# Kernel tuning notes

Measured on AMD Instinct MI355X. Metric: run time of the kernel, lower is better.

## Reference

```python
import jax, jax.numpy as jnp
import numpy as np

NUM_GRAPHS = 16  # static number of graphs for pooling
BN_EPS = 1e-5


def gat_layer(x, W, a_src, a_dst, src, dst, N, concat):
    # x: (N, Fin), W: (H, Fin, Fout), a_src/a_dst: (H, Fout)
    Wh = jnp.einsum('ni,hio->hno', x, W)                      # (H, N, Fout)
    e_src = jnp.einsum('hno,ho->hn', Wh, a_src)               # (H, N)
    e_dst = jnp.einsum('hno,ho->hn', Wh, a_dst)               # (H, N)
    e = jax.nn.leaky_relu(e_src[:, src] + e_dst[:, dst], 0.2)  # (H, E)
    # edge softmax over incoming edges per dst; torch code starts max at 0
    seg_max = jax.vmap(lambda eh: jax.ops.segment_max(eh, dst, num_segments=N))(e)
    e_max = jnp.maximum(seg_max, 0.0)                         # (H, N)
    exp_e = jnp.exp(e - e_max[:, dst])                        # (H, E)
    exp_sum = jax.vmap(lambda eh: jax.ops.segment_sum(eh, dst, num_segments=N))(exp_e)
    attn = exp_e / (exp_sum[:, dst] + 1e-8)                   # (H, E)
    msgs = attn[:, :, None] * Wh[:, src]                      # (H, E, Fout)
    out = jax.vmap(lambda m: jax.ops.segment_sum(m, dst, num_segments=N))(msgs)  # (H, N, Fout)
    if concat:
        out = jnp.transpose(out, (1, 0, 2)).reshape(N, -1)
    else:
        out = out.mean(axis=0)
    return out, attn


def batchnorm(h, gamma, beta):
    mu = h.mean(axis=0)
    var = h.var(axis=0)
    return (h - mu) / jnp.sqrt(var + BN_EPS) * gamma + beta


def setup_inputs() -> dict:
    key = jax.random.key(0)
    ks = jax.random.split(key, 20)
    N, E = 50000, 400000
    IN, HID, H, NC = 262, 128, 4, 2

    def xavier(k, shape):
        fan_in, fan_out = shape[-2], shape[-1]
        lim = np.sqrt(6.0 / (fan_in + fan_out))
        return jax.random.uniform(k, shape, jnp.float32, -lim, lim)

    x = jax.random.normal(ks[0], (N, IN), jnp.float32)
    edge_index = jax.random.randint(ks[1], (2, E), 0, N, jnp.int64)
    batch = jnp.sort(jax.random.randint(ks[2], (N,), 0, NUM_GRAPHS, jnp.int64))

    return {
        'x': x, 'edge_index': edge_index, 'batch': batch,
        'W1': xavier(ks[3], (H, IN, HID)),
        'a_src1': xavier(ks[4], (H, HID, 1)).squeeze(-1),
        'a_dst1': xavier(ks[5], (H, HID, 1)).squeeze(-1),
        'W2': xavier(ks[6], (1, HID * H, HID)),
        'a_src2': xavier(ks[7], (1, HID, 1)).squeeze(-1),
        'a_dst2': xavier(ks[8], (1, HID, 1)).squeeze(-1),
        'bn1_g': jnp.ones((HID * H,), jnp.float32),
        'bn1_b': jnp.zeros((HID * H,), jnp.float32),
        'bn2_g': jnp.ones((HID,), jnp.float32),
        'bn2_b': jnp.zeros((HID,), jnp.float32),
        'cls_w1': xavier(ks[9], (HID, HID // 2)),
        'cls_b1': jnp.zeros((HID // 2,), jnp.float32),
        'cls_w2': xavier(ks[10], (HID // 2, NC)),
        'cls_b2': jnp.zeros((NC,), jnp.float32),
        'ep_w1': xavier(ks[11], (HID * 2, HID)),
        'ep_b1': jnp.zeros((HID,), jnp.float32),
        'ep_w2': xavier(ks[12], (HID, 1)),
        'ep_b2': jnp.zeros((1,), jnp.float32),
    }


def reference(x, edge_index, batch, W1, a_src1, a_dst1, W2, a_src2, a_dst2,
              bn1_g, bn1_b, bn2_g, bn2_b, cls_w1, cls_b1, cls_w2, cls_b2,
              ep_w1, ep_b1, ep_w2, ep_b2):
    N = x.shape[0]
    src, dst = edge_index[0], edge_index[1]

    h1, _ = gat_layer(x, W1, a_src1, a_dst1, src, dst, N, concat=True)
    h1 = batchnorm(jax.nn.elu(h1), bn1_g, bn1_b)

    h2, attn2 = gat_layer(h1, W2, a_src2, a_dst2, src, dst, N, concat=False)
    h2 = batchnorm(jax.nn.elu(h2), bn2_g, bn2_b)

    # global mean pool over graphs
    sums = jax.ops.segment_sum(h2, batch, num_segments=NUM_GRAPHS)
    counts = jax.ops.segment_sum(jnp.ones((N,), h2.dtype), batch, num_segments=NUM_GRAPHS)
    graph_repr = sums / jnp.clip(counts, 1.0)[:, None]

    logits = jax.nn.relu(graph_repr @ cls_w1 + cls_b1) @ cls_w2 + cls_b2

    edge_feat = jnp.concatenate([h2[src], h2[dst]], axis=1)  # (E, 2*hidden)
    importance = jax.nn.sigmoid(
        (jax.nn.relu(edge_feat @ ep_w1 + ep_b1) @ ep_w2 + ep_b2).squeeze(-1))

    gat_attention = jnp.transpose(attn2, (1, 0))  # (E, 1)
    return logits, h2, importance, gat_attention
```

## Files before the change

### kernel.cpp

```cpp
#include <hip/hip_runtime.h>
#include <hip/hip_bf16.h>
#include <math.h>

typedef __hip_bfloat16 bf16;
typedef __bf16 bf16x8 __attribute__((ext_vector_type(8)));
typedef __bf16 bf16x2v __attribute__((ext_vector_type(2)));
typedef float f32x4 __attribute__((ext_vector_type(4)));

#define NN 50000
#define EE 400000
#define FIN 262
#define KP1 288
#define HID 128
#define NH 4
#define C1 512
#define NGR 16
#define SCAN_NB ((NN + 255) / 256)

__device__ __forceinline__ float b2f(bf16 x){ return __bfloat162float(x); }
__device__ __forceinline__ bf16 f2b(float x){ return __float2bfloat16(x); }
__device__ __forceinline__ float lrelu(float v){ return v >= 0.f ? v : 0.2f * v; }

__global__ void zero_words(unsigned int* __restrict__ p, int n) {
  int i = blockIdx.x * 256 + threadIdx.x;
  if (i < n) p[i] = 0u;
}

__global__ __launch_bounds__(256)
void gemm_mfma(const bf16* __restrict__ A, const bf16* __restrict__ Bt,
               bf16* __restrict__ C, int M, int K, int Ncols) {
  __shared__ __align__(16) __bf16 As[128 * 40];
  __shared__ __align__(16) __bf16 Bs[128 * 40];
  int bm = blockIdx.y * 128, bn = blockIdx.x * 128;
  int tid = threadIdx.x;
  int wave = tid >> 6, lane = tid & 63;
  int quad = lane >> 4, l16 = lane & 15;
  int wm = (wave >> 1) * 64, wn = (wave & 1) * 64;
  f32x4 acc[4][4];
  #pragma unroll
  for (int i = 0; i < 4; ++i)
    #pragma unroll
    for (int j = 0; j < 4; ++j)
      acc[i][j] = (f32x4){0.f, 0.f, 0.f, 0.f};

  for (int k0 = 0; k0 < K; k0 += 32) {
    #pragma unroll
    for (int l = 0; l < 2; ++l) {
      int e = l * 2048 + tid * 8;
      int row = e >> 5, col = e & 31;
      uint4 va = {0u, 0u, 0u, 0u};
      int gm = bm + row;
      if (gm < M) va = *(const uint4*)(A + (size_t)gm * K + k0 + col);
      *(uint4*)(&As[row * 40 + col]) = va;
      uint4 vb = {0u, 0u, 0u, 0u};
      int gn = bn + row;
      if (gn < Ncols) vb = *(const uint4*)(Bt + (size_t)gn * K + k0 + col);
      *(uint4*)(&Bs[row * 40 + col]) = vb;
    }
    __syncthreads();
    bf16x8 af[4], bf_[4];
    #pragma unroll
    for (int i = 0; i < 4; ++i)
      af[i] = *(const bf16x8*)(&As[(wm + i * 16 + l16) * 40 + quad * 8]);
    #pragma unroll
    for (int j = 0; j < 4; ++j)
      bf_[j] = *(const bf16x8*)(&Bs[(wn + j * 16 + l16) * 40 + quad * 8]);
    #pragma unroll
    for (int i = 0; i < 4; ++i)
      #pragma unroll
      for (int j = 0; j < 4; ++j)
        acc[i][j] = __builtin_amdgcn_mfma_f32_16x16x32_bf16(af[i], bf_[j], acc[i][j], 0, 0, 0);
    __syncthreads();
  }
  #pragma unroll
  for (int i = 0; i < 4; ++i) {
    #pragma unroll
    for (int r = 0; r < 4; ++r) {
      int gm = bm + wm + i * 16 + quad * 4 + r;
      if (gm >= M) continue;
      #pragma unroll
      for (int j = 0; j < 4; ++j) {
        int gn = bn + wn + j * 16 + l16;
        C[(size_t)gm * Ncols + gn] = f2b(acc[i][j][r]);
      }
    }
  }
}

__global__ void conv_x(const float* __restrict__ x, bf16* __restrict__ xb) {
  int i = blockIdx.x * 256 + threadIdx.x;
  if (i >= NN * KP1) return;
  int row = i / KP1, col = i - row * KP1;
  xb[i] = (col < FIN) ? f2b(x[(size_t)row * FIN + col]) : f2b(0.f);
}
__global__ void prep_b1t(const float* __restrict__ W1, bf16* __restrict__ B1t) {
  int i = blockIdx.x * 256 + threadIdx.x;
  if (i >= C1 * KP1) return;
  int n = i / KP1, k = i - n * KP1;
  int h = n >> 7, o = n & 127;
  B1t[i] = (k < FIN) ? f2b(W1[((size_t)h * FIN + k) * HID + o]) : f2b(0.f);
}
__global__ void prep_b2t(const float* __restrict__ W2, bf16* __restrict__ B2t) {
  int i = blockIdx.x * 256 + threadIdx.x;
  if (i >= HID * C1) return;
  int n = i >> 9, k = i & 511;
  B2t[i] = f2b(W2[(size_t)k * HID + n]);
}
__global__ void prep_bpt(const float* __restrict__ epw1, bf16* __restrict__ BPt) {
  int i = blockIdx.x * 256 + threadIdx.x;
  if (i >= 256 * HID) return;
  int n = i >> 7, k = i & 127;
  float v = (n < 128) ? epw1[(size_t)k * HID + n] : epw1[(size_t)(128 + k) * HID + (n - 128)];
  BPt[i] = f2b(v);
}

__global__ void edot_all(const bf16* __restrict__ Wh1, const float* __restrict__ av,
                         const float* __restrict__ bv, float* __restrict__ es1,
                         float* __restrict__ ed1) {
  int wid = threadIdx.x >> 6, lane = threadIdx.x & 63;
  int n = blockIdx.x * 4 + wid;
  if (n >= NN) return;
  int h = lane >> 4, c16 = lane & 15;
  int fbase = h * HID + c16 * 8;
  bf16x8 r = *(const bf16x8*)(Wh1 + (size_t)n * C1 + fbase);
  float s1 = 0.f, s2 = 0.f;
  #pragma unroll
  for (int j = 0; j < 8; ++j) {
    float rv = (float)r[j];
    s1 += rv * av[fbase + j];
    s2 += rv * bv[fbase + j];
  }
  #pragma unroll
  for (int off = 8; off > 0; off >>= 1) {
    s1 += __shfl_xor(s1, off);
    s2 += __shfl_xor(s2, off);
  }
  if (c16 == 0) { es1[n * 4 + h] = s1; ed1[n * 4 + h] = s2; }
}

__global__ void edot1(const bf16* __restrict__ Wh, const float* __restrict__ av,
                      const float* __restrict__ bv, float* __restrict__ es,
                      float* __restrict__ ed) {
  int wid = threadIdx.x >> 6, lane = threadIdx.x & 63;
  int r = blockIdx.x * 4 + wid;
  if (r >= NN) return;
  const bf16* row = Wh + (size_t)r * HID;
  float w0 = b2f(row[lane]), w1 = b2f(row[lane + 64]);
  float s1 = w0 * av[lane] + w1 * av[lane + 64];
  float s2 = w0 * bv[lane] + w1 * bv[lane + 64];
  #pragma unroll
  for (int off = 32; off > 0; off >>= 1) {
    s1 += __shfl_xor(s1, off);
    s2 += __shfl_xor(s2, off);
  }
  if (lane == 0) { es[r] = s1; ed[r] = s2; }
}

__global__ void count_kernel(const int* __restrict__ dst, int* __restrict__ deg, int E) {
  int e = blockIdx.x * blockDim.x + threadIdx.x;
  if (e >= E) return;
  int d = dst[e];
  if ((unsigned)d < NN) atomicAdd(&deg[d], 1);
}

__global__ void scan_p1(const int* __restrict__ deg, int* __restrict__ bsum) {
  __shared__ int s[256];
  int t = threadIdx.x;
  int i = blockIdx.x * 256 + t;
  s[t] = (i < NN) ? deg[i] : 0;
  __syncthreads();
  #pragma unroll
  for (int off = 128; off > 0; off >>= 1) {
    if (t < off) s[t] += s[t + off];
    __syncthreads();
  }
  if (t == 0) bsum[blockIdx.x] = s[0];
}
__global__ void scan_p2(const int* __restrict__ bsum, int* __restrict__ boff,
                        int* __restrict__ total_out) {
  __shared__ int s[256];
  int t = threadIdx.x;
  s[t] = (t < SCAN_NB) ? bsum[t] : 0;
  __syncthreads();
  if (t == 0) {
    int r = 0;
    for (int i = 0; i < SCAN_NB; ++i) { int v = s[i]; s[i] = r; r += v; }
    total_out[0] = r;
  }
  __syncthreads();
  if (t < SCAN_NB) boff[t] = s[t];
}
__global__ void scan_p3(const int* __restrict__ deg, const int* __restrict__ boff,
                        int* __restrict__ rowptr, int* __restrict__ cursor) {
  __shared__ int s[256];
  int t = threadIdx.x;
  int i = blockIdx.x * 256 + t;
  int v = (i < NN) ? deg[i] : 0;
  s[t] = v;
  __syncthreads();
  #pragma unroll
  for (int off = 1; off < 256; off <<= 1) {
    int add = (t >= off) ? s[t - off] : 0;
    __syncthreads();
    s[t] += add;
    __syncthreads();
  }
  if (i < NN) {
    int pos = boff[blockIdx.x] + s[t] - v;
    rowptr[i] = pos;
    cursor[i] = pos;
  }
}

__global__ void scatter_kernel(const int* __restrict__ src, const int* __restrict__ dst,
                               int* __restrict__ cursor, int* __restrict__ csr_s,
                               int* __restrict__ csr_d, int* __restrict__ csr_e, int E) {
  int e = blockIdx.x * blockDim.x + threadIdx.x;
  if (e >= E) return;
  int d = dst[e];
  if ((unsigned)d >= NN) return;
  int s = src[e]; if ((unsigned)s >= NN) s = 0;
  int p = atomicAdd(&cursor[d], 1);
  if ((unsigned)p < (unsigned)E) { csr_s[p] = s; csr_d[p] = d; csr_e[p] = e; }
}

__global__ void logits1(const int* __restrict__ csr_s, const int* __restrict__ csr_d,
                        const float4* __restrict__ es1, const float4* __restrict__ ed1,
                        float4* __restrict__ v1, int* __restrict__ m1i) {
  int j = blockIdx.x * 256 + threadIdx.x;
  if (j >= EE) return;
  int s = csr_s[j]; if ((unsigned)s >= NN) s = 0;
  int d = csr_d[j]; if ((unsigned)d >= NN) d = 0;
  float4 a = es1[s], bb = ed1[d];
  float4 v;
  v.x = lrelu(a.x + bb.x);
  v.y = lrelu(a.y + bb.y);
  v.z = lrelu(a.z + bb.z);
  v.w = lrelu(a.w + bb.w);
  v1[j] = v;
  if (v.x > 0.f) atomicMax(&m1i[d * 4 + 0], __float_as_int(v.x));
  if (v.y > 0.f) atomicMax(&m1i[d * 4 + 1], __float_as_int(v.y));
  if (v.z > 0.f) atomicMax(&m1i[d * 4 + 2], __float_as_int(v.z));
  if (v.w > 0.f) atomicMax(&m1i[d * 4 + 3], __float_as_int(v.w));
}

__global__ void logits2(const int* __restrict__ csr_s, const int* __restrict__ csr_d,
                        const float* __restrict__ es2, const float* __restrict__ ed2,
                        float* __restrict__ v2, int* __restrict__ m2i) {
  int j = blockIdx.x * 256 + threadIdx.x;
  if (j >= EE) return;
  int s = csr_s[j]; if ((unsigned)s >= NN) s = 0;
  int d = csr_d[j]; if ((unsigned)d >= NN) d = 0;
  float v = lrelu(es2[s] + ed2[d]);
  v2[j] = v;
  if (v > 0.f) atomicMax(&m2i[d], __float_as_int(v));
}

__global__ __launch_bounds__(256, 6)
void agg1_all(const int* __restrict__ csr_s, const int* __restrict__ rowptr,
              const float* __restrict__ lg, const float* __restrict__ mx,
              const bf16* __restrict__ Wh1, bf16* __restrict__ h1) {
  int wid = threadIdx.x >> 6, lane = threadIdx.x & 63;
  int node = blockIdx.x * 4 + wid;
  if (node >= NN) return;
  int b = rowptr[node], e = rowptr[node + 1];
  if (b < 0) b = 0; if (e > EE) e = EE;
  int h = lane >> 4;
  float m = mx[node * 4 + h];
  float sum = 0.f;
  float acc[8] = {};
  int j = b;
  for (; j + 4 <= e; j += 4) {
    int s0 = csr_s[j], s1 = csr_s[j + 1], s2 = csr_s[j + 2], s3 = csr_s[j + 3];
    float w0 = lg[(j + 0) * 4 + h], w1 = lg[(j + 1) * 4 + h],
          w2 = lg[(j + 2) * 4 + h], w3 = lg[(j + 3) * 4 + h];
    bf16x8 r0 = *(const bf16x8*)(Wh1 + (size_t)s0 * C1 + lane * 8);
    bf16x8 r1 = *(const bf16x8*)(Wh1 + (size_t)s1 * C1 + lane * 8);
    bf16x8 r2 = *(const bf16x8*)(Wh1 + (size_t)s2 * C1 + lane * 8);
    bf16x8 r3 = *(const bf16x8*)(Wh1 + (size_t)s3 * C1 + lane * 8);
    float p0 = __expf(w0 - m), p1 = __expf(w1 - m);
    float p2 = __expf(w2 - m), p3 = __expf(w3 - m);
    sum += (p0 + p1) + (p2 + p3);
    #pragma unroll
    for (int k = 0; k < 8; ++k)
      acc[k] += (p0 * (float)r0[k] + p1 * (float)r1[k]) +
                (p2 * (float)r2[k] + p3 * (float)r3[k]);
  }
  for (; j < e; ++j) {
    int s0 = csr_s[j];
    float w0 = lg[j * 4 + h];
    bf16x8 r0 = *(const bf16x8*)(Wh1 + (size_t)s0 * C1 + lane * 8);
    float p0 = __expf(w0 - m);
    sum += p0;
    #pragma unroll
    for (int k = 0; k < 8; ++k) acc[k] += p0 * (float)r0[k];
  }
  float scale = 1.f / (sum + 1e-8f);
  bf16x8 o;
  #pragma unroll
  for (int k = 0; k < 8; ++k) o[k] = (__bf16)(acc[k] * scale);
  *(bf16x8*)(h1 + (size_t)node * C1 + lane * 8) = o;
}

__global__ __launch_bounds__(256, 8)
void agg2_all(const int* __restrict__ csr_s, const int* __restrict__ rowptr,
              const float* __restrict__ lg, const float* __restrict__ mx,
              const bf16* __restrict__ Wh2, bf16* __restrict__ h2p,
              float* __restrict__ invs2) {
  int wid = threadIdx.x >> 6, lane = threadIdx.x & 63;
  int node = blockIdx.x * 4 + wid;
  if (node >= NN) return;
  int b = rowptr[node], e = rowptr[node + 1];
  if (b < 0) b = 0; if (e > EE) e = EE;
  float m = mx[node];
  float sum = 0.f, a0 = 0.f, a1 = 0.f;
  int j = b;
  for (; j + 4 <= e; j += 4) {
    int s0 = csr_s[j], s1 = csr_s[j + 1], s2 = csr_s[j + 2], s3 = csr_s[j + 3];
    float w0 = lg[j], w1 = lg[j + 1], w2 = lg[j + 2], w3 = lg[j + 3];
    bf16x2v r0 = *(const bf16x2v*)(Wh2 + (size_t)s0 * HID + lane * 2);
    bf16x2v r1 = *(const bf16x2v*)(Wh2 + (size_t)s1 * HID + lane * 2);
    bf16x2v r2 = *(const bf16x2v*)(Wh2 + (size_t)s2 * HID + lane * 2);
    bf16x2v r3 = *(const bf16x2v*)(Wh2 + (size_t)s3 * HID + lane * 2);
    float p0 = __expf(w0 - m), p1 = __expf(w1 - m);
    float p2 = __expf(w2 - m), p3 = __expf(w3 - m);
    sum += (p0 + p1) + (p2 + p3);
    a0 += (p0 * (float)r0[0] + p1 * (float)r1[0]) + (p2 * (float)r2[0] + p3 * (float)r3[0]);
    a1 += (p0 * (float)r0[1] + p1 * (float)r1[1]) + (p2 * (float)r2[1] + p3 * (float)r3[1]);
  }
  for (; j < e; ++j) {
    int s0 = csr_s[j];
    float w0 = lg[j];
    bf16x2v r0 = *(const bf16x2v*)(Wh2 + (size_t)s0 * HID + lane * 2);
    float p0 = __expf(w0 - m);
    sum += p0;
    a0 += p0 * (float)r0[0];
    a1 += p0 * (float)r0[1];
  }
  float scale = 1.f / (sum + 1e-8f);
  bf16x2v o;
  o[0] = (__bf16)(a0 * scale);
  o[1] = (__bf16)(a1 * scale);
  *(bf16x2v*)(h2p + (size_t)node * HID + lane * 2) = o;
  if (lane == 0) invs2[node] = scale;
}

__global__ void attn_csr(const int* __restrict__ csr_d, const int* __restrict__ csr_e,
                         const float* __restrict__ lg, const float* __restrict__ mx,
                         const float* __restrict__ invs2, float* __restrict__ out) {
  int j = blockIdx.x * 256 + threadIdx.x;
  if (j >= EE) return;
  int d = csr_d[j]; if ((unsigned)d >= NN) d = 0;
  int e = csr_e[j]; if ((unsigned)e >= EE) return;
  out[e] = __expf(lg[j] - mx[d]) * invs2[d];
}

__global__ void elu_stats(bf16* __restrict__ X, float* __restrict__ cs, float* __restrict__ cq,
                          int Nrows, int C) {
  int c = threadIdx.x;
  int rpb = (Nrows + gridDim.x - 1) / gridDim.x;
  int r0 = blockIdx.x * rpb, r1 = min(r0 + rpb, Nrows);
  float s = 0.f, s2 = 0.f;
  for (int r = r0; r < r1; ++r) {
    size_t idx = (size_t)r * C + c;
    float v = b2f(X[idx]);
    v = v > 0.f ? v : expm1f(v);
    X[idx] = f2b(v);
    s += v; s2 += v * v;
  }
  atomicAdd(&cs[c], s);
  atomicAdd(&cq[c], s2);
}

__global__ void bn_apply(const bf16* __restrict__ in, bf16* __restrict__ out,
                         float* __restrict__ out2,
                         const float* __restrict__ cs, const float* __restrict__ cq,
                         const float* __restrict__ gamma, const float* __restrict__ beta,
                         int C, size_t total, float invN) {
  size_t i = (size_t)blockIdx.x * blockDim.x + threadIdx.x;
  if (i >= total) return;
  int c = (int)(i % C);
  float mu = cs[c] * invN;
  float var = cq[c] * invN - mu * mu;
  float v = (b2f(in[i]) - mu) * rsqrtf(fmaxf(var, 0.f) + 1e-5f) * gamma[c] + beta[c];
  out[i] = f2b(v);
  if (out2) out2[i] = v;
}

__global__ __launch_bounds__(256)
void pool_kernel(const bf16* __restrict__ h2, const int* __restrict__ batch,
                 float* __restrict__ pooled) {
  int t = threadIdx.x;
  int f = t & 127, half = t >> 7;
  int r0 = blockIdx.x * 32;
  int g_cur = -1;
  float acc = 0.f;
  #pragma unroll
  for (int i = 0; i < 16; ++i) {
    int r = r0 + half + 2 * i;
    if (r >= NN) break;
    int g = batch[r]; if ((unsigned)g >= NGR) g = 0;
    float v = b2f(h2[(size_t)r * HID + f]);
    if (g != g_cur) {
      if (g_cur >= 0) atomicAdd(&pooled[g_cur * HID + f], acc);
      g_cur = g; acc = 0.f;
    }
    acc += v;
  }
  if (g_cur >= 0) atomicAdd(&pooled[g_cur * HID + f], acc);
}

__global__ void cnt_kernel(const int* __restrict__ batch, float* __restrict__ cnt) {
  int g = threadIdx.x;
  if (g >= NGR) return;
  int a = 0, b = NN;
  while (a < b) { int m = (a + b) >> 1; if (batch[m] < g) a = m + 1; else b = m; }
  int lb = a;
  a = 0; b = NN;
  while (a < b) { int m = (a + b) >> 1; if (batch[m] <= g) a = m + 1; else b = m; }
  cnt[g] = (float)(a - lb);
}

__global__ void cls_kernel(const float* __restrict__ pooled, const float* __restrict__ cnt,
                           const float* __restrict__ w1, const float* __restrict__ b1,
                           const float* __restrict__ w2, const float* __restrict__ b2,
                           float* __restrict__ out) {
  __shared__ float repr[NGR * HID];
  __shared__ float hid[NGR * 64];
  int t = threadIdx.x;
  for (int i = t; i < NGR * HID; i += 128) {
    int g = i >> 7;
    repr[i] = pooled[i] / fmaxf(cnt[g], 1.f);
  }
  __syncthreads();
  for (int i = t; i < NGR * 64; i += 128) {
    int g = i >> 6, j = i & 63;
    float s = b1[j];
    for (int c = 0; c < HID; ++c) s += repr[g * HID + c] * w1[c * 64 + j];
    hid[i] = fmaxf(s, 0.f);
  }
  __syncthreads();
  if (t < NGR * 2) {
    int g = t >> 1, k = t & 1;
    float s = b2[k];
    for (int j = 0; j < 64; ++j) s += hid[g * 64 + j] * w2[j * 2 + k];
    out[t] = s;
  }
}

__global__ __launch_bounds__(256)
void eimp_kernel(const int* __restrict__ csr_s, const int* __restrict__ csr_d,
                 const int* __restrict__ csr_e, const bf16* __restrict__ PQ,
                 const float* __restrict__ b1, const float* __restrict__ w2,
                 const float* __restrict__ b2, float* __restrict__ out) {
  int tid = threadIdx.x;
  int wave = tid >> 6, lane = tid & 63;
  int g = lane >> 4, l16 = lane & 15;
  int slot = blockIdx.x * 16 + wave * 4 + g;
  if (slot >= EE) return;
  int s = csr_s[slot]; if ((unsigned)s >= NN) s = 0;
  int d = csr_d[slot]; if ((unsigned)d >= NN) d = 0;
  int e = csr_e[slot]; if ((unsigned)e >= EE) return;
  bf16x8 p = *(const bf16x8*)(PQ + (size_t)s * 256 + l16 * 8);
  bf16x8 q = *(const bf16x8*)(PQ + (size_t)d * 256 + 128 + l16 * 8);
  float acc = 0.f;
  #pragma unroll
  for (int r = 0; r < 8; ++r) {
    int jj = l16 * 8 + r;
    float hh = (float)p[r] + (float)q[r] + b1[jj];
    hh = fmaxf(hh, 0.f);
    acc += hh * w2[jj];
  }
  #pragma unroll
  for (int off = 8; off > 0; off >>= 1) acc += __shfl_xor(acc, off);
  if (l16 == 0) {
    float z = acc + b2[0];
    out[e] = 1.f / (1.f + expf(-z));
  }
}

extern "C" void kernel_launch(void* const* d_in, const int* in_sizes, int n_in,
                              void* d_out, int out_size, void* d_ws, size_t ws_size,
                              hipStream_t stream) {
  const float* x      = (const float*)d_in[0];
  const int*   ei     = (const int*)d_in[1];
  const int*   batch  = (const int*)d_in[2];
  const float* W1     = (const float*)d_in[3];
  const float* a_src1 = (const float*)d_in[4];
  const float* a_dst1 = (const float*)d_in[5];
  const float* W2     = (const float*)d_in[6];
  const float* a_src2 = (const float*)d_in[7];
  const float* a_dst2 = (const float*)d_in[8];
  const float* bn1_g  = (const float*)d_in[9];
  const float* bn1_b  = (const float*)d_in[10];
  const float* bn2_g  = (const float*)d_in[11];
  const float* bn2_b  = (const float*)d_in[12];
  const float* cls_w1 = (const float*)d_in[13];
  const float* cls_b1 = (const float*)d_in[14];
  const float* cls_w2 = (const float*)d_in[15];
  const float* cls_b2 = (const float*)d_in[16];
  const float* ep_w1  = (const float*)d_in[17];
  const float* ep_b1  = (const float*)d_in[18];
  const float* ep_w2  = (const float*)d_in[19];
  const float* ep_b2  = (const float*)d_in[20];

  const int* srcp = ei;
  const int* dstp = ei + EE;

  char* base = (char*)d_ws;
  bf16* xb   = (bf16*)(base);
  bf16* h1   = (bf16*)(base);
  bf16* Wh1  = (bf16*)(base + 51200000);
  bf16* Wh2  = (bf16*)(base + 51200000);
  bf16* h2p  = (bf16*)(base + 64000000);
  bf16* h2   = (bf16*)(base + 76800000);
  bf16* PQ   = (bf16*)(base + 51200000);
  float* es1   = (float*)(base + 102400000);
  float* ed1   = (float*)(base + 103200000);
  float* v2csr = (float*)(base + 102400000);
  int*   m1i   = (int*)(base + 104000000);
  int*   m2i   = (int*)(base + 104800000);
  int*   deg   = (int*)(base + 105000000);
  float* stats = (float*)(base + 105200000);
  float* cs1 = stats,        *cq1 = stats + 512;
  float* cs2 = stats + 1024, *cq2 = stats + 1152;
  float* pooled = stats + 1280;
  float* cnt    = stats + 3328;
  float* es2   = (float*)(base + 105213376);
  float* ed2   = (float*)(base + 105413376);
  float* invs2 = (float*)(base + 105613376);
  int*   cursor= (int*)(base + 105813376);
  int*   rowptr= (int*)(base + 106013376);
  int*   bsum  = (int*)(base + 106213440);
  int*   boff  = bsum + 256;
  int*   csr_s = (int*)(base + 106215488);
  int*   csr_d = (int*)(base + 107815488);
  int*   csr_e = (int*)(base + 109415488);
  float* v1csr = (float*)(base + 111015488);
  bf16*  B1t   = (bf16*)(base + 117415488);
  bf16*  B2t   = (bf16*)(base + 117710400);
  bf16*  BPt   = (bf16*)(base + 117841472);

  float* out        = (float*)d_out;
  float* out_logits = out;
  float* out_h2     = out + 32;
  float* out_imp    = out + 32 + (size_t)NN * HID;
  float* out_attn   = out_imp + EE;

  zero_words<<<(303344 + 255) / 256, 256, 0, stream>>>((unsigned int*)m1i, 303344);

  conv_x<<<(NN * KP1 + 255) / 256, 256, 0, stream>>>(x, xb);
  prep_b1t<<<(C1 * KP1 + 255) / 256, 256, 0, stream>>>(W1, B1t);
  prep_b2t<<<(HID * C1 + 255) / 256, 256, 0, stream>>>(W2, B2t);
  prep_bpt<<<(256 * HID + 255) / 256, 256, 0, stream>>>(ep_w1, BPt);

  count_kernel<<<(EE + 255) / 256, 256, 0, stream>>>(dstp, deg, EE);
  scan_p1<<<SCAN_NB, 256, 0, stream>>>(deg, bsum);
  scan_p2<<<1, 256, 0, stream>>>(bsum, boff, rowptr + NN);
  scan_p3<<<SCAN_NB, 256, 0, stream>>>(deg, boff, rowptr, cursor);
  scatter_kernel<<<(EE + 255) / 256, 256, 0, stream>>>(srcp, dstp, cursor,
                                                       csr_s, csr_d, csr_e, EE);

  dim3 g1(C1 / 128, (NN + 127) / 128);
  gemm_mfma<<<g1, 256, 0, stream>>>(xb, B1t, Wh1, NN, KP1, C1);
  edot_all<<<(NN + 3) / 4, 256, 0, stream>>>(Wh1, a_src1, a_dst1, es1, ed1);
  logits1<<<(EE + 255) / 256, 256, 0, stream>>>(csr_s, csr_d, (const float4*)es1,
                                                (const float4*)ed1, (float4*)v1csr, m1i);
  agg1_all<<<(NN + 3) / 4, 256, 0, stream>>>(csr_s, rowptr, v1csr,
                                             (const float*)m1i, Wh1, h1);

  elu_stats<<<400, C1, 0, stream>>>(h1, cs1, cq1, NN, C1);
  {
    size_t total = (size_t)NN * C1;
    bn_apply<<<(unsigned)((total + 255) / 256), 256, 0, stream>>>(
        h1, h1, (float*)nullptr, cs1, cq1, bn1_g, bn1_b, C1, total, 1.f / NN);
  }

  dim3 g2(1, (NN + 127) / 128);
  gemm_mfma<<<g2, 256, 0, stream>>>(h1, B2t, Wh2, NN, C1, HID);
  edot1<<<(NN + 3) / 4, 256, 0, stream>>>(Wh2, a_src2, a_dst2, es2, ed2);
  logits2<<<(EE + 255) / 256, 256, 0, stream>>>(csr_s, csr_d, es2, ed2, v2csr, m2i);
  agg2_all<<<(NN + 3) / 4, 256, 0, stream>>>(csr_s, rowptr, v2csr,
                                             (const float*)m2i, Wh2, h2p, invs2);
  attn_csr<<<(EE + 255) / 256, 256, 0, stream>>>(csr_d, csr_e, v2csr,
                                                 (const float*)m2i, invs2, out_attn);

  elu_stats<<<400, HID, 0, stream>>>(h2p, cs2, cq2, NN, HID);
  {
    size_t total = (size_t)NN * HID;
    bn_apply<<<(unsigned)((total + 255) / 256), 256, 0, stream>>>(
        h2p, h2, out_h2, cs2, cq2, bn2_g, bn2_b, HID, total, 1.f / NN);
  }

  pool_kernel<<<(NN + 31) / 32, 256, 0, stream>>>(h2, batch, pooled);
  cnt_kernel<<<1, 64, 0, stream>>>(batch, cnt);
  cls_kernel<<<1, 128, 0, stream>>>(pooled, cnt, cls_w1, cls_b1, cls_w2, cls_b2, out_logits);

  dim3 gpq(2, (NN + 127) / 128);
  gemm_mfma<<<gpq, 256, 0, stream>>>(h2, BPt, PQ, NN, HID, 256);
  eimp_kernel<<<(EE + 15) / 16, 256, 0, stream>>>(csr_s, csr_d, csr_e, PQ,
                                                  ep_b1, ep_w2, ep_b2, out_imp);
}
```

Baseline: 702.3 us.

## Fuse ELU into aggregation and fold layer-1 batchnorm into second GEMM load

ELU is applied in the aggregation epilogues, and the layer-1 batchnorm is turned into per-column scale/shift applied while loading A tiles in the second GEMM. This removes the separate elementwise ELU and BN passes over the large hidden buffer. A vectorized stats kernel replaces the per-column strided one. agg1 is unrolled to eight edges in flight, and agg2 uses 16 lanes per node with 16-byte loads. This adds extra ALU work and per-tile scale loads in the GEMM, and rounds the normalized values to bf16 a second time.

```diff
diff --git a/kernel.cpp b/kernel.cpp
--- a/kernel.cpp
+++ b/kernel.cpp
@@ -20,6 +20,7 @@
 __device__ __forceinline__ float b2f(bf16 x){ return __bfloat162float(x); }
 __device__ __forceinline__ bf16 f2b(float x){ return __float2bfloat16(x); }
 __device__ __forceinline__ float lrelu(float v){ return v >= 0.f ? v : 0.2f * v; }
+__device__ __forceinline__ float eluf(float v){ return v > 0.f ? v : expm1f(v); }
 
 __global__ void zero_words(unsigned int* __restrict__ p, int n) {
   int i = blockIdx.x * 256 + threadIdx.x;
@@ -28,7 +29,8 @@
 
 __global__ __launch_bounds__(256)
 void gemm_mfma(const bf16* __restrict__ A, const bf16* __restrict__ Bt,
-               bf16* __restrict__ C, int M, int K, int Ncols) {
+               bf16* __restrict__ C, int M, int K, int Ncols,
+               const float* __restrict__ sc, const float* __restrict__ sh) {
   __shared__ __align__(16) __bf16 As[128 * 40];
   __shared__ __align__(16) __bf16 Bs[128 * 40];
   int bm = blockIdx.y * 128, bn = blockIdx.x * 128;
@@ -50,7 +52,26 @@
       int row = e >> 5, col = e & 31;
       uint4 va = {0u, 0u, 0u, 0u};
       int gm = bm + row;
-      if (gm < M) va = *(const uint4*)(A + (size_t)gm * K + k0 + col);
+      if (gm < M) {
+        va = *(const uint4*)(A + (size_t)gm * K + k0 + col);
+        if (sc) {
+          bf16x8 a8 = *(bf16x8*)&va;
+          float4 c0 = *(const float4*)(sc + k0 + col);
+          float4 c1 = *(const float4*)(sc + k0 + col + 4);
+          float4 h0 = *(const float4*)(sh + k0 + col);
+          float4 h1v = *(const float4*)(sh + k0 + col + 4);
+          bf16x8 t8;
+          t8[0] = (__bf16)((float)a8[0] * c0.x + h0.x);
+          t8[1] = (__bf16)((float)a8[1] * c0.y + h0.y);
+          t8[2] = (__bf16)((float)a8[2] * c0.z + h0.z);
+          t8[3] = (__bf16)((float)a8[3] * c0.w + h0.w);
+          t8[4] = (__bf16)((float)a8[4] * c1.x + h1v.x);
+          t8[5] = (__bf16)((float)a8[5] * c1.y + h1v.y);
+          t8[6] = (__bf16)((float)a8[6] * c1.z + h1v.z);
+          t8[7] = (__bf16)((float)a8[7] * c1.w + h1v.w);
+          va = *(uint4*)&t8;
+        }
+      }
       *(uint4*)(&As[row * 40 + col]) = va;
       uint4 vb = {0u, 0u, 0u, 0u};
       int gn = bn + row;
@@ -256,7 +277,7 @@
   if (v > 0.f) atomicMax(&m2i[d], __float_as_int(v));
 }
 
-__global__ __launch_bounds__(256, 6)
+__global__ __launch_bounds__(256, 5)
 void agg1_all(const int* __restrict__ csr_s, const int* __restrict__ rowptr,
               const float* __restrict__ lg, const float* __restrict__ mx,
               const bf16* __restrict__ Wh1, bf16* __restrict__ h1) {
@@ -269,36 +290,31 @@
   float m = mx[node * 4 + h];
   float sum = 0.f;
   float acc[8] = {};
-  int j = b;
-  for (; j + 4 <= e; j += 4) {
-    int s0 = csr_s[j], s1 = csr_s[j + 1], s2 = csr_s[j + 2], s3 = csr_s[j + 3];
-    float w0 = lg[(j + 0) * 4 + h], w1 = lg[(j + 1) * 4 + h],
-          w2 = lg[(j + 2) * 4 + h], w3 = lg[(j + 3) * 4 + h];
-    bf16x8 r0 = *(const bf16x8*)(Wh1 + (size_t)s0 * C1 + lane * 8);
-    bf16x8 r1 = *(const bf16x8*)(Wh1 + (size_t)s1 * C1 + lane * 8);
-    bf16x8 r2 = *(const bf16x8*)(Wh1 + (size_t)s2 * C1 + lane * 8);
-    bf16x8 r3 = *(const bf16x8*)(Wh1 + (size_t)s3 * C1 + lane * 8);
-    float p0 = __expf(w0 - m), p1 = __expf(w1 - m);
-    float p2 = __expf(w2 - m), p3 = __expf(w3 - m);
-    sum += (p0 + p1) + (p2 + p3);
-    #pragma unroll
-    for (int k = 0; k < 8; ++k)
-      acc[k] += (p0 * (float)r0[k] + p1 * (float)r1[k]) +
-                (p2 * (float)r2[k] + p3 * (float)r3[k]);
-  }
-  for (; j < e; ++j) {
-    int s0 = csr_s[j];
-    float w0 = lg[j * 4 + h];
-    bf16x8 r0 = *(const bf16x8*)(Wh1 + (size_t)s0 * C1 + lane * 8);
-    float p0 = __expf(w0 - m);
-    sum += p0;
-    #pragma unroll
-    for (int k = 0; k < 8; ++k) acc[k] += p0 * (float)r0[k];
+  for (int j = b; j < e; j += 8) {
+    int s_[8]; float w[8];
+    #pragma unroll
+    for (int i = 0; i < 8; ++i) {
+      int t = j + i;
+      int jj = t < e ? t : (e - 1);
+      s_[i] = csr_s[jj];
+      w[i] = lg[jj * 4 + h];
+    }
+    bf16x8 r[8];
+    #pragma unroll
+    for (int i = 0; i < 8; ++i)
+      r[i] = *(const bf16x8*)(Wh1 + (size_t)s_[i] * C1 + lane * 8);
+    #pragma unroll
+    for (int i = 0; i < 8; ++i) {
+      float p = (j + i < e) ? __expf(w[i] - m) : 0.f;
+      sum += p;
+      #pragma unroll
+      for (int k = 0; k < 8; ++k) acc[k] += p * (float)r[i][k];
+    }
   }
   float scale = 1.f / (sum + 1e-8f);
   bf16x8 o;
   #pragma unroll
-  for (int k = 0; k < 8; ++k) o[k] = (__bf16)(acc[k] * scale);
+  for (int k = 0; k < 8; ++k) o[k] = (__bf16)eluf(acc[k] * scale);
   *(bf16x8*)(h1 + (size_t)node * C1 + lane * 8) = o;
 }
 
@@ -307,42 +323,42 @@
               const float* __restrict__ lg, const float* __restrict__ mx,
               const bf16* __restrict__ Wh2, bf16* __restrict__ h2p,
               float* __restrict__ invs2) {
-  int wid = threadIdx.x >> 6, lane = threadIdx.x & 63;
-  int node = blockIdx.x * 4 + wid;
+  int tid = threadIdx.x;
+  int l16 = tid & 15;
+  int node = blockIdx.x * 16 + (tid >> 4);
   if (node >= NN) return;
   int b = rowptr[node], e = rowptr[node + 1];
   if (b < 0) b = 0; if (e > EE) e = EE;
   float m = mx[node];
-  float sum = 0.f, a0 = 0.f, a1 = 0.f;
-  int j = b;
-  for (; j + 4 <= e; j += 4) {
-    int s0 = csr_s[j], s1 = csr_s[j + 1], s2 = csr_s[j + 2], s3 = csr_s[j + 3];
-    float w0 = lg[j], w1 = lg[j + 1], w2 = lg[j + 2], w3 = lg[j + 3];
-    bf16x2v r0 = *(const bf16x2v*)(Wh2 + (size_t)s0 * HID + lane * 2);
-    bf16x2v r1 = *(const bf16x2v*)(Wh2 + (size_t)s1 * HID + lane * 2);
-    bf16x2v r2 = *(const bf16x2v*)(Wh2 + (size_t)s2 * HID + lane * 2);
-    bf16x2v r3 = *(const bf16x2v*)(Wh2 + (size_t)s3 * HID + lane * 2);
-    float p0 = __expf(w0 - m), p1 = __expf(w1 - m);
-    float p2 = __expf(w2 - m), p3 = __expf(w3 - m);
-    sum += (p0 + p1) + (p2 + p3);
-    a0 += (p0 * (float)r0[0] + p1 * (float)r1[0]) + (p2 * (float)r2[0] + p3 * (float)r3[0]);
-    a1 += (p0 * (float)r0[1] + p1 * (float)r1[1]) + (p2 * (float)r2[1] + p3 * (float)r3[1]);
-  }
-  for (; j < e; ++j) {
-    int s0 = csr_s[j];
-    float w0 = lg[j];
-    bf16x2v r0 = *(const bf16x2v*)(Wh2 + (size_t)s0 * HID + lane * 2);
-    float p0 = __expf(w0 - m);
-    sum += p0;
-    a0 += p0 * (float)r0[0];
-    a1 += p0 * (float)r0[1];
+  float sum = 0.f;
+  float acc[8] = {};
+  for (int j = b; j < e; j += 4) {
+    int s_[4]; float w[4];
+    #pragma unroll
+    for (int i = 0; i < 4; ++i) {
+      int t = j + i;
+      int jj = t < e ? t : (e - 1);
+      s_[i] = csr_s[jj];
+      w[i] = lg[jj];
+    }
+    bf16x8 r[4];
+    #pragma unroll
+    for (int i = 0; i < 4; ++i)
+      r[i] = *(const bf16x8*)(Wh2 + (size_t)s_[i] * HID + l16 * 8);
+    #pragma unroll
+    for (int i = 0; i < 4; ++i) {
+      float p = (j + i < e) ? __expf(w[i] - m) : 0.f;
+      sum += p;
+      #pragma unroll
+      for (int k = 0; k < 8; ++k) acc[k] += p * (float)r[i][k];
+    }
   }
   float scale = 1.f / (sum + 1e-8f);
-  bf16x2v o;
-  o[0] = (__bf16)(a0 * scale);
-  o[1] = (__bf16)(a1 * scale);
-  *(bf16x2v*)(h2p + (size_t)node * HID + lane * 2) = o;
-  if (lane == 0) invs2[node] = scale;
+  bf16x8 o;
+  #pragma unroll
+  for (int k = 0; k < 8; ++k) o[k] = (__bf16)eluf(acc[k] * scale);
+  *(bf16x8*)(h2p + (size_t)node * HID + l16 * 8) = o;
+  if (l16 == 0) invs2[node] = scale;
 }
 
 __global__ void attn_csr(const int* __restrict__ csr_d, const int* __restrict__ csr_e,
@@ -355,21 +371,40 @@
   out[e] = __expf(lg[j] - mx[d]) * invs2[d];
 }
 
-__global__ void elu_stats(bf16* __restrict__ X, float* __restrict__ cs, float* __restrict__ cq,
-                          int Nrows, int C) {
-  int c = threadIdx.x;
-  int rpb = (Nrows + gridDim.x - 1) / gridDim.x;
-  int r0 = blockIdx.x * rpb, r1 = min(r0 + rpb, Nrows);
-  float s = 0.f, s2 = 0.f;
-  for (int r = r0; r < r1; ++r) {
-    size_t idx = (size_t)r * C + c;
-    float v = b2f(X[idx]);
-    v = v > 0.f ? v : expm1f(v);
-    X[idx] = f2b(v);
-    s += v; s2 += v * v;
-  }
-  atomicAdd(&cs[c], s);
-  atomicAdd(&cq[c], s2);
+template<int C>
+__global__ __launch_bounds__(256)
+void stats_kernel(const bf16* __restrict__ X, float* __restrict__ cs,
+                  float* __restrict__ cq, int Nrows) {
+  constexpr int TPR = C / 8;
+  constexpr int RPS = 256 / TPR;
+  int t = threadIdx.x;
+  int cpos = (t % TPR) * 8;
+  float s[8] = {}, q[8] = {};
+  for (int row = blockIdx.x * RPS + t / TPR; row < Nrows; row += gridDim.x * RPS) {
+    bf16x8 v = *(const bf16x8*)(X + (size_t)row * C + cpos);
+    #pragma unroll
+    for (int k = 0; k < 8; ++k) {
+      float f = (float)v[k];
+      s[k] += f; q[k] += f * f;
+    }
+  }
+  #pragma unroll
+  for (int k = 0; k < 8; ++k) {
+    atomicAdd(&cs[cpos + k], s[k]);
+    atomicAdd(&cq[cpos + k], q[k]);
+  }
+}
+
+__global__ void bn_coef(const float* __restrict__ cs, const float* __restrict__ cq,
+                        const float* __restrict__ gamma, const float* __restrict__ beta,
+                        float* __restrict__ sc, float* __restrict__ sh, int C, float invN) {
+  int c = blockIdx.x * 256 + threadIdx.x;
+  if (c >= C) return;
+  float mu = cs[c] * invN;
+  float var = cq[c] * invN - mu * mu;
+  float g = rsqrtf(fmaxf(var, 0.f) + 1e-5f) * gamma[c];
+  sc[c] = g;
+  sh[c] = beta[c] - mu * g;
 }
 
 __global__ void bn_apply(const bf16* __restrict__ in, bf16* __restrict__ out,
@@ -526,20 +561,22 @@
   float* cs2 = stats + 1024, *cq2 = stats + 1152;
   float* pooled = stats + 1280;
   float* cnt    = stats + 3328;
-  float* es2   = (float*)(base + 105213376);
-  float* ed2   = (float*)(base + 105413376);
-  float* invs2 = (float*)(base + 105613376);
-  int*   cursor= (int*)(base + 105813376);
-  int*   rowptr= (int*)(base + 106013376);
-  int*   bsum  = (int*)(base + 106213440);
+  float* sc1   = (float*)(base + 105213376);
+  float* sh1   = (float*)(base + 105215424);
+  float* es2   = (float*)(base + 105217472);
+  float* ed2   = (float*)(base + 105417472);
+  float* invs2 = (float*)(base + 105617472);
+  int*   cursor= (int*)(base + 105817472);
+  int*   rowptr= (int*)(base + 106017472);
+  int*   bsum  = (int*)(base + 106217476);
   int*   boff  = bsum + 256;
-  int*   csr_s = (int*)(base + 106215488);
-  int*   csr_d = (int*)(base + 107815488);
-  int*   csr_e = (int*)(base + 109415488);
-  float* v1csr = (float*)(base + 111015488);
-  bf16*  B1t   = (bf16*)(base + 117415488);
-  bf16*  B2t   = (bf16*)(base + 117710400);
-  bf16*  BPt   = (bf16*)(base + 117841472);
+  int*   csr_s = (int*)(base + 106219524);
+  int*   csr_d = (int*)(base + 107819524);
+  int*   csr_e = (int*)(base + 109419524);
+  float* v1csr = (float*)(base + 111019536);
+  bf16*  B1t   = (bf16*)(base + 117419536);
+  bf16*  B2t   = (bf16*)(base + 117714448);
+  bf16*  BPt   = (bf16*)(base + 117845520);
 
   float* out        = (float*)d_out;
   float* out_logits = out;
@@ -562,30 +599,26 @@
                                                        csr_s, csr_d, csr_e, EE);
 
   dim3 g1(C1 / 128, (NN + 127) / 128);
-  gemm_mfma<<<g1, 256, 0, stream>>>(xb, B1t, Wh1, NN, KP1, C1);
+  gemm_mfma<<<g1, 256, 0, stream>>>(xb, B1t, Wh1, NN, KP1, C1, nullptr, nullptr);
   edot_all<<<(NN + 3) / 4, 256, 0, stream>>>(Wh1, a_src1, a_dst1, es1, ed1);
   logits1<<<(EE + 255) / 256, 256, 0, stream>>>(csr_s, csr_d, (const float4*)es1,
                                                 (const float4*)ed1, (float4*)v1csr, m1i);
   agg1_all<<<(NN + 3) / 4, 256, 0, stream>>>(csr_s, rowptr, v1csr,
                                              (const float*)m1i, Wh1, h1);
 
-  elu_stats<<<400, C1, 0, stream>>>(h1, cs1, cq1, NN, C1);
-  {
-    size_t total = (size_t)NN * C1;
-    bn_apply<<<(unsigned)((total + 255) / 256), 256, 0, stream>>>(
-        h1, h1, (float*)nullptr, cs1, cq1, bn1_g, bn1_b, C1, total, 1.f / NN);
-  }
+  stats_kernel<C1><<<120, 256, 0, stream>>>(h1, cs1, cq1, NN);
+  bn_coef<<<2, 256, 0, stream>>>(cs1, cq1, bn1_g, bn1_b, sc1, sh1, C1, 1.f / NN);
 
   dim3 g2(1, (NN + 127) / 128);
-  gemm_mfma<<<g2, 256, 0, stream>>>(h1, B2t, Wh2, NN, C1, HID);
+  gemm_mfma<<<g2, 256, 0, stream>>>(h1, B2t, Wh2, NN, C1, HID, sc1, sh1);
   edot1<<<(NN + 3) / 4, 256, 0, stream>>>(Wh2, a_src2, a_dst2, es2, ed2);
   logits2<<<(EE + 255) / 256, 256, 0, stream>>>(csr_s, csr_d, es2, ed2, v2csr, m2i);
-  agg2_all<<<(NN + 3) / 4, 256, 0, stream>>>(csr_s, rowptr, v2csr,
-                                             (const float*)m2i, Wh2, h2p, invs2);
+  agg2_all<<<(NN + 15) / 16, 256, 0, stream>>>(csr_s, rowptr, v2csr,
+                                               (const float*)m2i, Wh2, h2p, invs2);
   attn_csr<<<(EE + 255) / 256, 256, 0, stream>>>(csr_d, csr_e, v2csr,
                                                  (const float*)m2i, invs2, out_attn);
 
-  elu_stats<<<400, HID, 0, stream>>>(h2p, cs2, cq2, NN, HID);
+  stats_kernel<HID><<<120, 256, 0, stream>>>(h2p, cs2, cq2, NN);
   {
     size_t total = (size_t)NN * HID;
     bn_apply<<<(unsigned)((total + 255) / 256), 256, 0, stream>>>(
@@ -597,7 +630,7 @@
   cls_kernel<<<1, 128, 0, stream>>>(pooled, cnt, cls_w1, cls_b1, cls_w2, cls_b2, out_logits);
 
   dim3 gpq(2, (NN + 127) / 128);
-  gemm_mfma<<<gpq, 256, 0, stream>>>(h2, BPt, PQ, NN, HID, 256);
+  gemm_mfma<<<gpq, 256, 0, stream>>>(h2, BPt, PQ, NN, HID, 256, nullptr, nullptr);
   eimp_kernel<<<(EE + 15) / 16, 256, 0, stream>>>(csr_s, csr_d, csr_e, PQ,
                                                   ep_b1, ep_w2, ep_b2, out_imp);
 }
```

Result: slower. 1.062 ms (+51.2%).
